# Performance work log

Hardware: AMD Instinct MI355X
Metric: run time of the kernel (lower is better)

Reference implementation:

```python
import jax, jax.numpy as jnp
import numpy as np

FEATURE_SIZES = [300, 1000, 1000, 500, 150, 12, 31, 30, 200, 50000, 50000, 20000, 100000]
# sections per table index i (from feature_sizes_dict -> feature_sections_dict in original)
SECTIONS = [(0, 1), (1, 2), (2, 3), (3, 4), (4, 5), (5, 6), (6, 7), (7, 10),
            (10, 24), (26, 28), (28, 30), (24, 26), (30, 45)]
N, F, E = 8192, 45, 256
_perm, _tbl = [], []
for _i, (_a, _b) in enumerate(SECTIONS):
    for _j in range(_a, _b):
        _perm.append(_j)
        _tbl.append(_i)
PERM = np.array(_perm)              # original Xi column for field position p (concat order)
TBL = np.array(_tbl)                # table index for field position p
OFFSETS = np.concatenate([[0], np.cumsum(FEATURE_SIZES)[:-1]]).astype(np.int32)
FIELD_OFF = OFFSETS[TBL]            # row offset into concatenated table per field position
TOTAL_V = int(np.sum(FEATURE_SIZES))  # 223273
VOCAB_COL = np.zeros(F, np.int32)
VOCAB_COL[PERM] = np.array(FEATURE_SIZES, np.int32)[TBL]  # per-column valid vocab for Xi


def setup_inputs() -> dict:
    key = jax.random.key(0)
    ks = jax.random.split(key, 10)
    Xi = jax.random.randint(ks[0], (N, F), 0, jnp.asarray(VOCAB_COL), dtype=jnp.int32)
    Xv = jax.random.uniform(ks[1], (N, F), dtype=jnp.float32)
    W1 = jax.random.normal(ks[2], (TOTAL_V, 1), dtype=jnp.float32) * 0.01
    W2 = jax.random.normal(ks[3], (TOTAL_V, E), dtype=jnp.float32) * 0.01
    bias = jax.random.normal(ks[4], (1,), dtype=jnp.float32)
    l1_w = jax.random.normal(ks[5], (32, F * E), dtype=jnp.float32) * 0.02
    l1_b = jnp.zeros((32,), jnp.float32)
    l2_w = jax.random.normal(ks[6], (32, 32), dtype=jnp.float32) * 0.02
    l2_b = jnp.zeros((32,), jnp.float32)
    return {"Xi": Xi, "Xv": Xv, "W1": W1, "W2": W2, "bias": bias,
            "l1_w": l1_w, "l1_b": l1_b, "bn1_g": jnp.ones((32,), jnp.float32),
            "bn1_b": jnp.zeros((32,), jnp.float32), "l2_w": l2_w, "l2_b": l2_b,
            "bn2_g": jnp.ones((32,), jnp.float32), "bn2_b": jnp.zeros((32,), jnp.float32)}


def _batchnorm(x, g, b, eps=1e-5):
    # training-mode BN: biased batch statistics (PyTorch normalization convention)
    m = x.mean(0)
    v = x.var(0)
    return (x - m) * jax.lax.rsqrt(v + eps) * g + b


def reference(Xi, Xv, W1, W2, bias, l1_w, l1_b, bn1_g, bn1_b, l2_w, l2_b, bn2_g, bn2_b):
    perm = jnp.asarray(PERM)
    foff = jnp.asarray(FIELD_OFF)
    idx = Xi[:, perm] + foff[None, :]          # (N, 45) rows into concatenated tables
    xv = Xv[:, perm]                            # (N, 45) values in concat order
    # first-order: scalar embedding * value per field
    fm_first = W1[idx, 0] * xv                  # (N, 45)
    # second-order: E-dim embedding * value per field
    e = W2[idx] * xv[:, :, None]                # (N, 45, E)
    s = e.sum(axis=1)                           # (N, E)
    fm_second = 0.5 * (s * s - (e * e).sum(axis=1))  # (N, E)
    # deep part (concat of per-field 2nd-order embs, in original loop order)
    deep = e.reshape(e.shape[0], -1)            # (N, 45*E)
    h = _batchnorm(deep @ l1_w.T + l1_b, bn1_g, bn1_b)
    h = _batchnorm(h @ l2_w.T + l2_b, bn2_g, bn2_b)  # (N, 32); no final num_classes linear in original
    return fm_first.sum(axis=1) + fm_second.sum(axis=1) + h.sum(axis=1) + bias  # (N,)
```

## Files before the change

kernel.cpp:

```cpp
#include <hip/hip_runtime.h>
#include <hip/hip_bf16.h>

#define NS 8192
#define NF 45
#define ED 256
#define L1K 11520
#define NH 32

typedef __attribute__((ext_vector_type(8))) short bf16x8;
typedef __attribute__((ext_vector_type(4))) float f32x4;

__constant__ int c_perm[NF] = {
    0,1,2,3,4,5,6,7,8,9,
    10,11,12,13,14,15,16,17,18,19,20,21,22,23,
    26,27, 28,29, 24,25,
    30,31,32,33,34,35,36,37,38,39,40,41,42,43,44};
__constant__ int c_foff[NF] = {
    0,300,1300,2300,2800,2950,2962,2993,2993,2993,
    3023,3023,3023,3023,3023,3023,3023,3023,3023,3023,3023,3023,3023,3023,
    3223,3223, 53223,53223, 103223,103223,
    123223,123223,123223,123223,123223,123223,123223,123223,
    123223,123223,123223,123223,123223,123223,123223};

__device__ __forceinline__ short f2bf(float x) {
    unsigned u = __builtin_bit_cast(unsigned, x);
    u += 0x7fffu + ((u >> 16) & 1u);
    return (short)(u >> 16);
}

__global__ __launch_bounds__(256) void k_prep(const int* __restrict__ Xi,
                                              const float* __restrict__ Xv,
                                              int* __restrict__ idxP,
                                              float* __restrict__ xvP) {
    int t = blockIdx.x * 256 + threadIdx.x;
    if (t >= NS * NF) return;
    unsigned n = (unsigned)t / NF;
    int f = t - (int)n * NF;
    int col = c_perm[f];
    idxP[t] = Xi[n * NF + col] + c_foff[f];
    xvP[t]  = Xv[n * NF + col];
}

__global__ __launch_bounds__(256) void k_pack(const float* __restrict__ l1w,
                                              short* __restrict__ bfrag) {
    int t = blockIdx.x * 256 + threadIdx.x;
    if (t >= NF * 8192) return;
    int i  = t & 7;
    int l  = (t >> 3) & 63;
    int nt = (t >> 9) & 1;
    int ks = (t >> 10) & 7;
    int f  = t >> 13;
    int kout = nt * 16 + (l & 15);
    int col  = f * 256 + ks * 32 + (l >> 4) * 8 + i;
    bfrag[t] = f2bf(l1w[kout * L1K + col]);
}

__global__ __launch_bounds__(256) void k_main(const float* __restrict__ W2,
                                              const float* __restrict__ W1,
                                              const int* __restrict__ idxP,
                                              const float* __restrict__ xvP,
                                              const short* __restrict__ bfrag,
                                              float* __restrict__ h1pre,
                                              float* __restrict__ partial) {
    __shared__ int   s_idx[16 * NF];
    __shared__ float s_xv [16 * NF];
    __shared__ float s_red[4 * 16 * NH];
    __shared__ float s_q[4][16];
    __shared__ float s_fm1[16];

    const int tid = threadIdx.x;
    const int w = tid >> 6;
    const int l = tid & 63;
    const int m = l & 15;
    const int g4 = l >> 4;
    const int n0 = blockIdx.x * 16;

    for (int t = tid; t < 16 * NF; t += 256) {
        s_idx[t] = idxP[n0 * NF + t];
        s_xv[t]  = xvP [n0 * NF + t];
    }
    __syncthreads();

    const int ks0 = w * 2;
    f32x4 acc0 = {0.f, 0.f, 0.f, 0.f};
    f32x4 acc1 = {0.f, 0.f, 0.f, 0.f};
    float sA[16];
    #pragma unroll
    for (int i = 0; i < 16; ++i) sA[i] = 0.f;
    float esq = 0.f, fm1 = 0.f;

    const short* bbase = bfrag + (size_t)(ks0 * 2) * 512 + l * 8;

    for (int f = 0; f < NF; ++f) {
        const int   idx = s_idx[m * NF + f];
        const float xv  = s_xv [m * NF + f];
        const float* wr = W2 + (size_t)idx * ED + ks0 * 32 + g4 * 8;

        f32x4 a0 = *(const f32x4*)(wr);
        f32x4 a1 = *(const f32x4*)(wr + 4);
        f32x4 a2 = *(const f32x4*)(wr + 32);
        f32x4 a3 = *(const f32x4*)(wr + 36);

        const short* bp = bbase + (size_t)f * 8192;
        bf16x8 b00 = *(const bf16x8*)(bp);
        bf16x8 b01 = *(const bf16x8*)(bp + 512);
        bf16x8 b10 = *(const bf16x8*)(bp + 1024);
        bf16x8 b11 = *(const bf16x8*)(bp + 1536);

        float e[16];
        e[0]=a0.x*xv; e[1]=a0.y*xv; e[2]=a0.z*xv; e[3]=a0.w*xv;
        e[4]=a1.x*xv; e[5]=a1.y*xv; e[6]=a1.z*xv; e[7]=a1.w*xv;
        e[8]=a2.x*xv; e[9]=a2.y*xv; e[10]=a2.z*xv; e[11]=a2.w*xv;
        e[12]=a3.x*xv; e[13]=a3.y*xv; e[14]=a3.z*xv; e[15]=a3.w*xv;

        #pragma unroll
        for (int i = 0; i < 16; ++i) { sA[i] += e[i]; esq += e[i] * e[i]; }

        bf16x8 af0, af1;
        #pragma unroll
        for (int i = 0; i < 8; ++i) { af0[i] = f2bf(e[i]); af1[i] = f2bf(e[8 + i]); }

        acc0 = __builtin_amdgcn_mfma_f32_16x16x32_bf16(af0, b00, acc0, 0, 0, 0);
        acc1 = __builtin_amdgcn_mfma_f32_16x16x32_bf16(af0, b01, acc1, 0, 0, 0);
        acc0 = __builtin_amdgcn_mfma_f32_16x16x32_bf16(af1, b10, acc0, 0, 0, 0);
        acc1 = __builtin_amdgcn_mfma_f32_16x16x32_bf16(af1, b11, acc1, 0, 0, 0);

        if (w == 0) fm1 += W1[idx] * xv;
    }

    float q = -esq;
    #pragma unroll
    for (int i = 0; i < 16; ++i) q += sA[i] * sA[i];
    q += __shfl_xor(q, 16);
    q += __shfl_xor(q, 32);
    if (l < 16) s_q[w][l] = q;
    if (w == 0 && l < 16) s_fm1[l] = fm1;

    #pragma unroll
    for (int r = 0; r < 4; ++r) {
        s_red[w * 512 + (g4 * 4 + r) * 32 +      m] = acc0[r];
        s_red[w * 512 + (g4 * 4 + r) * 32 + 16 + m] = acc1[r];
    }
    __syncthreads();

    for (int t = tid; t < 512; t += 256) {
        float v = s_red[t] + s_red[512 + t] + s_red[1024 + t] + s_red[1536 + t];
        int s = t >> 5, k = t & 31;
        h1pre[(size_t)(n0 + s) * NH + k] = v;
    }
    if (tid < 16) {
        float fm2 = 0.5f * (s_q[0][tid] + s_q[1][tid] + s_q[2][tid] + s_q[3][tid]);
        partial[n0 + tid] = s_fm1[tid] + fm2;
    }
}

__global__ __launch_bounds__(256) void k_stats(const float* __restrict__ h1pre,
                                               float* __restrict__ S1,
                                               float* __restrict__ S2) {
    __shared__ float hc[128 * NH];
    const int tid = threadIdx.x;
    const int base = blockIdx.x * 128;
    for (int t = tid; t < 128 * NH; t += 256) hc[t] = h1pre[(size_t)base * NH + t];
    __syncthreads();

    const int j = tid >> 3;
    const int ks = (tid & 7) * 4;
    float a0 = 0.f, a1 = 0.f, a2 = 0.f, a3 = 0.f;
    for (int n = 0; n < 128; ++n) {
        float hj = hc[n * NH + j];
        f32x4 h = *(const f32x4*)&hc[n * NH + ks];
        a0 += hj * h.x; a1 += hj * h.y; a2 += hj * h.z; a3 += hj * h.w;
    }
    atomicAdd(&S2[j * NH + ks + 0], a0);
    atomicAdd(&S2[j * NH + ks + 1], a1);
    atomicAdd(&S2[j * NH + ks + 2], a2);
    atomicAdd(&S2[j * NH + ks + 3], a3);
    if (tid < NH) {
        float s = 0.f;
        for (int n = 0; n < 128; ++n) s += hc[n * NH + tid];
        atomicAdd(&S1[tid], s);
    }
}

__global__ __launch_bounds__(256) void k_coef(const float* __restrict__ S1,
                                              const float* __restrict__ S2,
                                              const float* __restrict__ g1,
                                              const float* __restrict__ l2w,
                                              const float* __restrict__ g2,
                                              const float* __restrict__ b2,
                                              const float* __restrict__ bias,
                                              float* __restrict__ cvec,
                                              float* __restrict__ k0out) {
    __shared__ float m1[NH], d1[NH], g2r2[NH], csh[NH];
    const int t = threadIdx.x;
    const float invN = 1.f / (float)NS;
    if (t < NH) {
        float mm = S1[t] * invN;
        float v1 = S2[t * NH + t] * invN - mm * mm;
        m1[t] = mm;
        d1[t] = g1[t] * rsqrtf(v1 + 1e-5f);
    }
    __syncthreads();
    if (t < NH) {
        float aw[NH];
        float p = 0.f;
        for (int j = 0; j < NH; ++j) { aw[j] = l2w[t * NH + j] * d1[j]; p += aw[j] * m1[j]; }
        float v2 = 0.f;
        for (int j = 0; j < NH; ++j) {
            float acc = 0.f;
            for (int j2 = 0; j2 < NH; ++j2) acc += aw[j2] * S2[j * NH + j2];
            v2 += aw[j] * acc;
        }
        v2 = v2 * invN - p * p;
        g2r2[t] = g2[t] * rsqrtf(v2 + 1e-5f);
    }
    __syncthreads();
    if (t < NH) {
        float s = 0.f;
        for (int k = 0; k < NH; ++k) s += g2r2[k] * l2w[k * NH + t];
        float c = d1[t] * s;
        csh[t] = c;
        cvec[t] = c;
    }
    __syncthreads();
    if (t == 0) {
        float k0 = bias[0];
        for (int k = 0; k < NH; ++k) k0 += b2[k];
        for (int j = 0; j < NH; ++j) k0 -= csh[j] * m1[j];
        k0out[0] = k0;
    }
}

__global__ __launch_bounds__(256) void k_final(const float* __restrict__ h1pre,
                                               const float* __restrict__ partial,
                                               const float* __restrict__ cvec,
                                               const float* __restrict__ k0p,
                                               float* __restrict__ out) {
    __shared__ float c[NH];
    __shared__ float k0s;
    const int t = threadIdx.x;
    if (t < NH) c[t] = cvec[t];
    if (t == 0) k0s = k0p[0];
    __syncthreads();
    const int n = blockIdx.x * 256 + t;
    const f32x4* hp = (const f32x4*)(h1pre + (size_t)n * NH);
    float dot = 0.f;
    #pragma unroll
    for (int q = 0; q < 8; ++q) {
        f32x4 h = hp[q];
        dot += h.x * c[q * 4] + h.y * c[q * 4 + 1] + h.z * c[q * 4 + 2] + h.w * c[q * 4 + 3];
    }
    out[n] = partial[n] + dot + k0s;
}

extern "C" void kernel_launch(void* const* d_in, const int* in_sizes, int n_in,
                              void* d_out, int out_size, void* d_ws, size_t ws_size,
                              hipStream_t stream) {
    const int*   Xi   = (const int*)  d_in[0];
    const float* Xv   = (const float*)d_in[1];
    const float* W1   = (const float*)d_in[2];
    const float* W2   = (const float*)d_in[3];
    const float* bias = (const float*)d_in[4];
    const float* l1w  = (const float*)d_in[5];
    const float* g1   = (const float*)d_in[7];
    const float* l2w  = (const float*)d_in[9];
    const float* g2   = (const float*)d_in[11];
    const float* b2   = (const float*)d_in[12];
    float* out = (float*)d_out;

    char* ws = (char*)d_ws;
    int*   idxP  = (int*)ws;
    float* xvP   = (float*)(ws + (size_t)368640 * 4);
    short* bfrag = (short*)(ws + (size_t)737280 * 4);
    float* h1    = (float*)(ws + (size_t)737280 * 4 + 737280);
    float* part  = h1 + (size_t)NS * NH;
    float* S1    = part + NS;
    float* S2    = S1 + NH;
    float* cvec  = S2 + NH * NH;
    float* k0p   = cvec + NH;

    hipMemsetAsync(S1, 0, (NH + NH * NH) * sizeof(float), stream);
    k_prep <<<(NS * NF + 255) / 256, 256, 0, stream>>>(Xi, Xv, idxP, xvP);
    k_pack <<<(NF * 8192 + 255) / 256, 256, 0, stream>>>(l1w, bfrag);
    k_main <<<NS / 16, 256, 0, stream>>>(W2, W1, idxP, xvP, bfrag, h1, part);
    k_stats<<<64, 256, 0, stream>>>(h1, S1, S2);
    k_coef <<<1, 256, 0, stream>>>(S1, S2, g1, l2w, g2, b2, bias, cvec, k0p);
    k_final<<<NS / 256, 256, 0, stream>>>(h1, part, cvec, k0p, out);
}
```

Baseline: 392.0 us.

## Fuse index prep into main kernel and split embedding dim across two blocks

Removes the separate k_prep kernel by gathering the permuted indices and values directly inside k_main. The main kernel now launches twice as many blocks, each covering half of the 256-wide embedding dimension, which halves per-thread register and load work and raises occupancy. The two halves write separate partial h1 and FM outputs that k_stats and k_final sum. The cost is redundant index gathering per half-block and extra reads of partial buffers downstream.

```diff
diff --git a/kernel.cpp b/kernel.cpp
--- a/kernel.cpp
+++ b/kernel.cpp
@@ -26,19 +26,6 @@
     unsigned u = __builtin_bit_cast(unsigned, x);
     u += 0x7fffu + ((u >> 16) & 1u);
     return (short)(u >> 16);
-}
-
-__global__ __launch_bounds__(256) void k_prep(const int* __restrict__ Xi,
-                                              const float* __restrict__ Xv,
-                                              int* __restrict__ idxP,
-                                              float* __restrict__ xvP) {
-    int t = blockIdx.x * 256 + threadIdx.x;
-    if (t >= NS * NF) return;
-    unsigned n = (unsigned)t / NF;
-    int f = t - (int)n * NF;
-    int col = c_perm[f];
-    idxP[t] = Xi[n * NF + col] + c_foff[f];
-    xvP[t]  = Xv[n * NF + col];
 }
 
 __global__ __launch_bounds__(256) void k_pack(const float* __restrict__ l1w,
@@ -57,80 +44,77 @@
 
 __global__ __launch_bounds__(256) void k_main(const float* __restrict__ W2,
                                               const float* __restrict__ W1,
-                                              const int* __restrict__ idxP,
-                                              const float* __restrict__ xvP,
+                                              const int* __restrict__ Xi,
+                                              const float* __restrict__ Xv,
                                               const short* __restrict__ bfrag,
-                                              float* __restrict__ h1pre,
-                                              float* __restrict__ partial) {
+                                              float* __restrict__ h1h,
+                                              float* __restrict__ parth) {
     __shared__ int   s_idx[16 * NF];
     __shared__ float s_xv [16 * NF];
     __shared__ float s_red[4 * 16 * NH];
     __shared__ float s_q[4][16];
     __shared__ float s_fm1[16];
 
-    const int tid = threadIdx.x;
-    const int w = tid >> 6;
-    const int l = tid & 63;
-    const int m = l & 15;
-    const int g4 = l >> 4;
-    const int n0 = blockIdx.x * 16;
+    const int tid  = threadIdx.x;
+    const int w    = tid >> 6;
+    const int l    = tid & 63;
+    const int m    = l & 15;
+    const int g4   = l >> 4;
+    const int half = blockIdx.x & 1;
+    const int n0   = (blockIdx.x >> 1) * 16;
+    const int ks   = half * 4 + w;
 
     for (int t = tid; t < 16 * NF; t += 256) {
-        s_idx[t] = idxP[n0 * NF + t];
-        s_xv[t]  = xvP [n0 * NF + t];
-    }
-    __syncthreads();
-
-    const int ks0 = w * 2;
+        int f = t % NF;
+        int n = n0 + t / NF;
+        int col = c_perm[f];
+        s_idx[t] = Xi[n * NF + col] + c_foff[f];
+        s_xv[t]  = Xv[n * NF + col];
+    }
+    __syncthreads();
+
     f32x4 acc0 = {0.f, 0.f, 0.f, 0.f};
     f32x4 acc1 = {0.f, 0.f, 0.f, 0.f};
-    float sA[16];
-    #pragma unroll
-    for (int i = 0; i < 16; ++i) sA[i] = 0.f;
+    float sA[8];
+    #pragma unroll
+    for (int i = 0; i < 8; ++i) sA[i] = 0.f;
     float esq = 0.f, fm1 = 0.f;
 
-    const short* bbase = bfrag + (size_t)(ks0 * 2) * 512 + l * 8;
+    const short* bbase = bfrag + (size_t)ks * 1024 + l * 8;
+    const float* wbase = W2 + ks * 32 + g4 * 8;
 
     for (int f = 0; f < NF; ++f) {
         const int   idx = s_idx[m * NF + f];
         const float xv  = s_xv [m * NF + f];
-        const float* wr = W2 + (size_t)idx * ED + ks0 * 32 + g4 * 8;
+        const float* wr = wbase + (size_t)idx * ED;
 
         f32x4 a0 = *(const f32x4*)(wr);
         f32x4 a1 = *(const f32x4*)(wr + 4);
-        f32x4 a2 = *(const f32x4*)(wr + 32);
-        f32x4 a3 = *(const f32x4*)(wr + 36);
 
         const short* bp = bbase + (size_t)f * 8192;
-        bf16x8 b00 = *(const bf16x8*)(bp);
-        bf16x8 b01 = *(const bf16x8*)(bp + 512);
-        bf16x8 b10 = *(const bf16x8*)(bp + 1024);
-        bf16x8 b11 = *(const bf16x8*)(bp + 1536);
-
-        float e[16];
+        bf16x8 b0 = *(const bf16x8*)(bp);
+        bf16x8 b1 = *(const bf16x8*)(bp + 512);
+
+        float e[8];
         e[0]=a0.x*xv; e[1]=a0.y*xv; e[2]=a0.z*xv; e[3]=a0.w*xv;
         e[4]=a1.x*xv; e[5]=a1.y*xv; e[6]=a1.z*xv; e[7]=a1.w*xv;
-        e[8]=a2.x*xv; e[9]=a2.y*xv; e[10]=a2.z*xv; e[11]=a2.w*xv;
-        e[12]=a3.x*xv; e[13]=a3.y*xv; e[14]=a3.z*xv; e[15]=a3.w*xv;
 
         #pragma unroll
-        for (int i = 0; i < 16; ++i) { sA[i] += e[i]; esq += e[i] * e[i]; }
-
-        bf16x8 af0, af1;
+        for (int i = 0; i < 8; ++i) { sA[i] += e[i]; esq += e[i] * e[i]; }
+
+        bf16x8 af;
         #pragma unroll
-        for (int i = 0; i < 8; ++i) { af0[i] = f2bf(e[i]); af1[i] = f2bf(e[8 + i]); }
-
-        acc0 = __builtin_amdgcn_mfma_f32_16x16x32_bf16(af0, b00, acc0, 0, 0, 0);
-        acc1 = __builtin_amdgcn_mfma_f32_16x16x32_bf16(af0, b01, acc1, 0, 0, 0);
-        acc0 = __builtin_amdgcn_mfma_f32_16x16x32_bf16(af1, b10, acc0, 0, 0, 0);
-        acc1 = __builtin_amdgcn_mfma_f32_16x16x32_bf16(af1, b11, acc1, 0, 0, 0);
-
-        if (w == 0) fm1 += W1[idx] * xv;
+        for (int i = 0; i < 8; ++i) af[i] = f2bf(e[i]);
+
+        acc0 = __builtin_amdgcn_mfma_f32_16x16x32_bf16(af, b0, acc0, 0, 0, 0);
+        acc1 = __builtin_amdgcn_mfma_f32_16x16x32_bf16(af, b1, acc1, 0, 0, 0);
+
+        if (half == 0 && w == 0) fm1 += W1[idx] * xv;
     }
 
     float q = -esq;
     #pragma unroll
-    for (int i = 0; i < 16; ++i) q += sA[i] * sA[i];
+    for (int i = 0; i < 8; ++i) q += sA[i] * sA[i];
     q += __shfl_xor(q, 16);
     q += __shfl_xor(q, 32);
     if (l < 16) s_q[w][l] = q;
@@ -143,24 +127,26 @@
     }
     __syncthreads();
 
+    float* h1out = h1h + (size_t)half * NS * NH;
     for (int t = tid; t < 512; t += 256) {
         float v = s_red[t] + s_red[512 + t] + s_red[1024 + t] + s_red[1536 + t];
         int s = t >> 5, k = t & 31;
-        h1pre[(size_t)(n0 + s) * NH + k] = v;
+        h1out[(size_t)(n0 + s) * NH + k] = v;
     }
     if (tid < 16) {
         float fm2 = 0.5f * (s_q[0][tid] + s_q[1][tid] + s_q[2][tid] + s_q[3][tid]);
-        partial[n0 + tid] = s_fm1[tid] + fm2;
-    }
-}
-
-__global__ __launch_bounds__(256) void k_stats(const float* __restrict__ h1pre,
+        parth[half * NS + n0 + tid] = s_fm1[tid] + fm2;
+    }
+}
+
+__global__ __launch_bounds__(256) void k_stats(const float* __restrict__ h1h,
                                                float* __restrict__ S1,
                                                float* __restrict__ S2) {
     __shared__ float hc[128 * NH];
     const int tid = threadIdx.x;
     const int base = blockIdx.x * 128;
-    for (int t = tid; t < 128 * NH; t += 256) hc[t] = h1pre[(size_t)base * NH + t];
+    for (int t = tid; t < 128 * NH; t += 256)
+        hc[t] = h1h[(size_t)base * NH + t] + h1h[(size_t)NS * NH + base * NH + t];
     __syncthreads();
 
     const int j = tid >> 3;
@@ -231,8 +217,8 @@
     }
 }
 
-__global__ __launch_bounds__(256) void k_final(const float* __restrict__ h1pre,
-                                               const float* __restrict__ partial,
+__global__ __launch_bounds__(256) void k_final(const float* __restrict__ h1h,
+                                               const float* __restrict__ parth,
                                                const float* __restrict__ cvec,
                                                const float* __restrict__ k0p,
                                                float* __restrict__ out) {
@@ -243,14 +229,17 @@
     if (t == 0) k0s = k0p[0];
     __syncthreads();
     const int n = blockIdx.x * 256 + t;
-    const f32x4* hp = (const f32x4*)(h1pre + (size_t)n * NH);
+    const f32x4* hp0 = (const f32x4*)(h1h + (size_t)n * NH);
+    const f32x4* hp1 = (const f32x4*)(h1h + (size_t)NS * NH + (size_t)n * NH);
     float dot = 0.f;
     #pragma unroll
     for (int q = 0; q < 8; ++q) {
-        f32x4 h = hp[q];
-        dot += h.x * c[q * 4] + h.y * c[q * 4 + 1] + h.z * c[q * 4 + 2] + h.w * c[q * 4 + 3];
-    }
-    out[n] = partial[n] + dot + k0s;
+        f32x4 h0 = hp0[q];
+        f32x4 h1 = hp1[q];
+        dot += (h0.x + h1.x) * c[q * 4]     + (h0.y + h1.y) * c[q * 4 + 1]
+             + (h0.z + h1.z) * c[q * 4 + 2] + (h0.w + h1.w) * c[q * 4 + 3];
+    }
+    out[n] = parth[n] + parth[NS + n] + dot + k0s;
 }
 
 extern "C" void kernel_launch(void* const* d_in, const int* in_sizes, int n_in,
@@ -269,21 +258,18 @@
     float* out = (float*)d_out;
 
     char* ws = (char*)d_ws;
-    int*   idxP  = (int*)ws;
-    float* xvP   = (float*)(ws + (size_t)368640 * 4);
-    short* bfrag = (short*)(ws + (size_t)737280 * 4);
-    float* h1    = (float*)(ws + (size_t)737280 * 4 + 737280);
-    float* part  = h1 + (size_t)NS * NH;
-    float* S1    = part + NS;
+    short* bfrag = (short*)ws;
+    float* h1h   = (float*)(ws + (size_t)368640 * 2);
+    float* parth = h1h + (size_t)2 * NS * NH;
+    float* S1    = parth + 2 * NS;
     float* S2    = S1 + NH;
     float* cvec  = S2 + NH * NH;
     float* k0p   = cvec + NH;
 
     hipMemsetAsync(S1, 0, (NH + NH * NH) * sizeof(float), stream);
-    k_prep <<<(NS * NF + 255) / 256, 256, 0, stream>>>(Xi, Xv, idxP, xvP);
     k_pack <<<(NF * 8192 + 255) / 256, 256, 0, stream>>>(l1w, bfrag);
-    k_main <<<NS / 16, 256, 0, stream>>>(W2, W1, idxP, xvP, bfrag, h1, part);
-    k_stats<<<64, 256, 0, stream>>>(h1, S1, S2);
+    k_main <<<NS / 16 * 2, 256, 0, stream>>>(W2, W1, Xi, Xv, bfrag, h1h, parth);
+    k_stats<<<64, 256, 0, stream>>>(h1h, S1, S2);
     k_coef <<<1, 256, 0, stream>>>(S1, S2, g1, l2w, g2, b2, bias, cvec, k0p);
-    k_final<<<NS / 256, 256, 0, stream>>>(h1, part, cvec, k0p, out);
-}
+    k_final<<<NS / 256, 256, 0, stream>>>(h1h, parth, cvec, k0p, out);
+}
```

After: 388.3 us. About the same (-0.9%).

## Fuse prep, stats, coef and final kernels into main pipeline

Applied to the files above, without the earlier changes.

Folds the index/value permutation into k_main's shared-memory load, computes the BN1 moment accumulations (S1/S2) inside k_main via atomics, and merges the coefficient and final-output kernels into one kernel where each block redundantly recomputes the BN coefficients. Zeroing of the accumulators moves into k_pack, and the bf16 conversion uses the packed v_cvt_pk_bf16_f32 instruction. This cuts launch count from six plus a memset down to three and removes intermediate idx/xv buffers. In exchange there are many more atomics (512 blocks instead of 64) and duplicated coefficient work in each of 32 blocks.

```diff
diff --git a/kernel.cpp b/kernel.cpp
--- a/kernel.cpp
+++ b/kernel.cpp
@@ -28,22 +28,19 @@
     return (short)(u >> 16);
 }
 
-__global__ __launch_bounds__(256) void k_prep(const int* __restrict__ Xi,
-                                              const float* __restrict__ Xv,
-                                              int* __restrict__ idxP,
-                                              float* __restrict__ xvP) {
+__device__ __forceinline__ unsigned pk_bf16(float a, float b) {
+    unsigned r;
+    asm("v_cvt_pk_bf16_f32 %0, %1, %2" : "=v"(r) : "v"(a), "v"(b));
+    return r;
+}
+
+__global__ __launch_bounds__(256) void k_pack(const float* __restrict__ l1w,
+                                              short* __restrict__ bfrag,
+                                              float* __restrict__ S1) {
     int t = blockIdx.x * 256 + threadIdx.x;
-    if (t >= NS * NF) return;
-    unsigned n = (unsigned)t / NF;
-    int f = t - (int)n * NF;
-    int col = c_perm[f];
-    idxP[t] = Xi[n * NF + col] + c_foff[f];
-    xvP[t]  = Xv[n * NF + col];
-}
-
-__global__ __launch_bounds__(256) void k_pack(const float* __restrict__ l1w,
-                                              short* __restrict__ bfrag) {
-    int t = blockIdx.x * 256 + threadIdx.x;
+    if (blockIdx.x == 0) {
+        for (int i = threadIdx.x; i < NH + NH * NH; i += 256) S1[i] = 0.f;
+    }
     if (t >= NF * 8192) return;
     int i  = t & 7;
     int l  = (t >> 3) & 63;
@@ -57,14 +54,17 @@
 
 __global__ __launch_bounds__(256) void k_main(const float* __restrict__ W2,
                                               const float* __restrict__ W1,
-                                              const int* __restrict__ idxP,
-                                              const float* __restrict__ xvP,
+                                              const int* __restrict__ Xi,
+                                              const float* __restrict__ Xv,
                                               const short* __restrict__ bfrag,
                                               float* __restrict__ h1pre,
-                                              float* __restrict__ partial) {
+                                              float* __restrict__ partial,
+                                              float* __restrict__ S1,
+                                              float* __restrict__ S2) {
     __shared__ int   s_idx[16 * NF];
     __shared__ float s_xv [16 * NF];
     __shared__ float s_red[4 * 16 * NH];
+    __shared__ float s_h[16 * NH];
     __shared__ float s_q[4][16];
     __shared__ float s_fm1[16];
 
@@ -76,8 +76,11 @@
     const int n0 = blockIdx.x * 16;
 
     for (int t = tid; t < 16 * NF; t += 256) {
-        s_idx[t] = idxP[n0 * NF + t];
-        s_xv[t]  = xvP [n0 * NF + t];
+        int f = t % NF;
+        int n = n0 + t / NF;
+        int col = c_perm[f];
+        s_idx[t] = Xi[n * NF + col] + c_foff[f];
+        s_xv[t]  = Xv[n * NF + col];
     }
     __syncthreads();
 
@@ -116,14 +119,20 @@
         #pragma unroll
         for (int i = 0; i < 16; ++i) { sA[i] += e[i]; esq += e[i] * e[i]; }
 
-        bf16x8 af0, af1;
-        #pragma unroll
-        for (int i = 0; i < 8; ++i) { af0[i] = f2bf(e[i]); af1[i] = f2bf(e[8 + i]); }
-
-        acc0 = __builtin_amdgcn_mfma_f32_16x16x32_bf16(af0, b00, acc0, 0, 0, 0);
-        acc1 = __builtin_amdgcn_mfma_f32_16x16x32_bf16(af0, b01, acc1, 0, 0, 0);
-        acc0 = __builtin_amdgcn_mfma_f32_16x16x32_bf16(af1, b10, acc0, 0, 0, 0);
-        acc1 = __builtin_amdgcn_mfma_f32_16x16x32_bf16(af1, b11, acc1, 0, 0, 0);
+        union { bf16x8 v; unsigned u[4]; } A0, A1;
+        A0.u[0] = pk_bf16(e[0],  e[1]);
+        A0.u[1] = pk_bf16(e[2],  e[3]);
+        A0.u[2] = pk_bf16(e[4],  e[5]);
+        A0.u[3] = pk_bf16(e[6],  e[7]);
+        A1.u[0] = pk_bf16(e[8],  e[9]);
+        A1.u[1] = pk_bf16(e[10], e[11]);
+        A1.u[2] = pk_bf16(e[12], e[13]);
+        A1.u[3] = pk_bf16(e[14], e[15]);
+
+        acc0 = __builtin_amdgcn_mfma_f32_16x16x32_bf16(A0.v, b00, acc0, 0, 0, 0);
+        acc1 = __builtin_amdgcn_mfma_f32_16x16x32_bf16(A0.v, b01, acc1, 0, 0, 0);
+        acc0 = __builtin_amdgcn_mfma_f32_16x16x32_bf16(A1.v, b10, acc0, 0, 0, 0);
+        acc1 = __builtin_amdgcn_mfma_f32_16x16x32_bf16(A1.v, b11, acc1, 0, 0, 0);
 
         if (w == 0) fm1 += W1[idx] * xv;
     }
@@ -145,58 +154,59 @@
 
     for (int t = tid; t < 512; t += 256) {
         float v = s_red[t] + s_red[512 + t] + s_red[1024 + t] + s_red[1536 + t];
-        int s = t >> 5, k = t & 31;
-        h1pre[(size_t)(n0 + s) * NH + k] = v;
+        h1pre[(size_t)n0 * NH + t] = v;
+        s_h[t] = v;
     }
     if (tid < 16) {
         float fm2 = 0.5f * (s_q[0][tid] + s_q[1][tid] + s_q[2][tid] + s_q[3][tid]);
         partial[n0 + tid] = s_fm1[tid] + fm2;
     }
-}
-
-__global__ __launch_bounds__(256) void k_stats(const float* __restrict__ h1pre,
-                                               float* __restrict__ S1,
-                                               float* __restrict__ S2) {
-    __shared__ float hc[128 * NH];
-    const int tid = threadIdx.x;
-    const int base = blockIdx.x * 128;
-    for (int t = tid; t < 128 * NH; t += 256) hc[t] = h1pre[(size_t)base * NH + t];
-    __syncthreads();
-
-    const int j = tid >> 3;
-    const int ks = (tid & 7) * 4;
-    float a0 = 0.f, a1 = 0.f, a2 = 0.f, a3 = 0.f;
-    for (int n = 0; n < 128; ++n) {
-        float hj = hc[n * NH + j];
-        f32x4 h = *(const f32x4*)&hc[n * NH + ks];
-        a0 += hj * h.x; a1 += hj * h.y; a2 += hj * h.z; a3 += hj * h.w;
-    }
-    atomicAdd(&S2[j * NH + ks + 0], a0);
-    atomicAdd(&S2[j * NH + ks + 1], a1);
-    atomicAdd(&S2[j * NH + ks + 2], a2);
-    atomicAdd(&S2[j * NH + ks + 3], a3);
-    if (tid < NH) {
-        float s = 0.f;
-        for (int n = 0; n < 128; ++n) s += hc[n * NH + tid];
-        atomicAdd(&S1[tid], s);
-    }
-}
-
-__global__ __launch_bounds__(256) void k_coef(const float* __restrict__ S1,
-                                              const float* __restrict__ S2,
-                                              const float* __restrict__ g1,
-                                              const float* __restrict__ l2w,
-                                              const float* __restrict__ g2,
-                                              const float* __restrict__ b2,
-                                              const float* __restrict__ bias,
-                                              float* __restrict__ cvec,
-                                              float* __restrict__ k0out) {
+    __syncthreads();
+
+    {
+        const int j  = tid >> 3;
+        const int k4 = (tid & 7) * 4;
+        float a0 = 0.f, a1 = 0.f, a2 = 0.f, a3 = 0.f;
+        #pragma unroll
+        for (int s = 0; s < 16; ++s) {
+            float hj = s_h[s * NH + j];
+            f32x4 h = *(const f32x4*)&s_h[s * NH + k4];
+            a0 += hj * h.x; a1 += hj * h.y; a2 += hj * h.z; a3 += hj * h.w;
+        }
+        atomicAdd(&S2[j * NH + k4 + 0], a0);
+        atomicAdd(&S2[j * NH + k4 + 1], a1);
+        atomicAdd(&S2[j * NH + k4 + 2], a2);
+        atomicAdd(&S2[j * NH + k4 + 3], a3);
+        if (tid < NH) {
+            float s1 = 0.f;
+            #pragma unroll
+            for (int s = 0; s < 16; ++s) s1 += s_h[s * NH + tid];
+            atomicAdd(&S1[tid], s1);
+        }
+    }
+}
+
+__global__ __launch_bounds__(256) void k_cf(const float* __restrict__ S1,
+                                            const float* __restrict__ S2,
+                                            const float* __restrict__ g1,
+                                            const float* __restrict__ l2w,
+                                            const float* __restrict__ g2,
+                                            const float* __restrict__ b2,
+                                            const float* __restrict__ bias,
+                                            const float* __restrict__ h1pre,
+                                            const float* __restrict__ partial,
+                                            float* __restrict__ out) {
+    __shared__ float sS2[NH * NH];
     __shared__ float m1[NH], d1[NH], g2r2[NH], csh[NH];
+    __shared__ float k0s;
     const int t = threadIdx.x;
     const float invN = 1.f / (float)NS;
+
+    for (int i = t; i < NH * NH; i += 256) sS2[i] = S2[i];
+    __syncthreads();
     if (t < NH) {
         float mm = S1[t] * invN;
-        float v1 = S2[t * NH + t] * invN - mm * mm;
+        float v1 = sS2[t * NH + t] * invN - mm * mm;
         m1[t] = mm;
         d1[t] = g1[t] * rsqrtf(v1 + 1e-5f);
     }
@@ -208,7 +218,7 @@
         float v2 = 0.f;
         for (int j = 0; j < NH; ++j) {
             float acc = 0.f;
-            for (int j2 = 0; j2 < NH; ++j2) acc += aw[j2] * S2[j * NH + j2];
+            for (int j2 = 0; j2 < NH; ++j2) acc += aw[j2] * sS2[j * NH + j2];
             v2 += aw[j] * acc;
         }
         v2 = v2 * invN - p * p;
@@ -218,37 +228,25 @@
     if (t < NH) {
         float s = 0.f;
         for (int k = 0; k < NH; ++k) s += g2r2[k] * l2w[k * NH + t];
-        float c = d1[t] * s;
-        csh[t] = c;
-        cvec[t] = c;
+        csh[t] = d1[t] * s;
     }
     __syncthreads();
     if (t == 0) {
         float k0 = bias[0];
         for (int k = 0; k < NH; ++k) k0 += b2[k];
         for (int j = 0; j < NH; ++j) k0 -= csh[j] * m1[j];
-        k0out[0] = k0;
-    }
-}
-
-__global__ __launch_bounds__(256) void k_final(const float* __restrict__ h1pre,
-                                               const float* __restrict__ partial,
-                                               const float* __restrict__ cvec,
-                                               const float* __restrict__ k0p,
-                                               float* __restrict__ out) {
-    __shared__ float c[NH];
-    __shared__ float k0s;
-    const int t = threadIdx.x;
-    if (t < NH) c[t] = cvec[t];
-    if (t == 0) k0s = k0p[0];
-    __syncthreads();
+        k0s = k0;
+    }
+    __syncthreads();
+
     const int n = blockIdx.x * 256 + t;
     const f32x4* hp = (const f32x4*)(h1pre + (size_t)n * NH);
     float dot = 0.f;
     #pragma unroll
     for (int q = 0; q < 8; ++q) {
         f32x4 h = hp[q];
-        dot += h.x * c[q * 4] + h.y * c[q * 4 + 1] + h.z * c[q * 4 + 2] + h.w * c[q * 4 + 3];
+        dot += h.x * csh[q * 4] + h.y * csh[q * 4 + 1]
+             + h.z * csh[q * 4 + 2] + h.w * csh[q * 4 + 3];
     }
     out[n] = partial[n] + dot + k0s;
 }
@@ -269,21 +267,13 @@
     float* out = (float*)d_out;
 
     char* ws = (char*)d_ws;
-    int*   idxP  = (int*)ws;
-    float* xvP   = (float*)(ws + (size_t)368640 * 4);
-    short* bfrag = (short*)(ws + (size_t)737280 * 4);
-    float* h1    = (float*)(ws + (size_t)737280 * 4 + 737280);
+    short* bfrag = (short*)ws;
+    float* h1    = (float*)(ws + (size_t)368640 * 2);
     float* part  = h1 + (size_t)NS * NH;
     float* S1    = part + NS;
     float* S2    = S1 + NH;
-    float* cvec  = S2 + NH * NH;
-    float* k0p   = cvec + NH;
-
-    hipMemsetAsync(S1, 0, (NH + NH * NH) * sizeof(float), stream);
-    k_prep <<<(NS * NF + 255) / 256, 256, 0, stream>>>(Xi, Xv, idxP, xvP);
-    k_pack <<<(NF * 8192 + 255) / 256, 256, 0, stream>>>(l1w, bfrag);
-    k_main <<<NS / 16, 256, 0, stream>>>(W2, W1, idxP, xvP, bfrag, h1, part);
-    k_stats<<<64, 256, 0, stream>>>(h1, S1, S2);
-    k_coef <<<1, 256, 0, stream>>>(S1, S2, g1, l2w, g2, b2, bias, cvec, k0p);
-    k_final<<<NS / 256, 256, 0, stream>>>(h1, part, cvec, k0p, out);
-}
+
+    k_pack<<<(NF * 8192 + 255) / 256, 256, 0, stream>>>(l1w, bfrag, S1);
+    k_main<<<NS / 16, 256, 0, stream>>>(W2, W1, Xi, Xv, bfrag, h1, part, S1, S2);
+    k_cf  <<<NS / 256, 256, 0, stream>>>(S1, S2, g1, l2w, g2, b2, bias, h1, part, out);
+}
```

Measured after the change: 412.5 us. +5.2%, slower.

## Stage gathered embeddings in LDS with double-buffered chunks and fuse prep into main

Applied to the files above, without the earlier changes.

The prep kernel is removed and its index permutation and offset work moves into k_main's prologue. Embedding rows are now gathered with fully coalesced 1KB row reads (one row per wave-iteration). Each row is scaled, converted to bf16 and written into a double-buffered LDS tile two fields at a time, and the MFMA loop reads its A fragments from LDS while the next chunk is prefetched. The aim is to replace scattered per-lane 32-byte gathers with contiguous row reads and overlap gather latency with compute. In exchange it adds a block barrier per phase, more LDS use, and computes the FM second-order sums from bf16-rounded values, which loses some precision.

```diff
diff --git a/kernel.cpp b/kernel.cpp
--- a/kernel.cpp
+++ b/kernel.cpp
@@ -6,6 +6,10 @@
 #define ED 256
 #define L1K 11520
 #define NH 32
+#define CHUNK 2
+#define NPH 23
+#define ROWSTRIDE 264
+#define FSTRIDE (16 * ROWSTRIDE)
 
 typedef __attribute__((ext_vector_type(8))) short bf16x8;
 typedef __attribute__((ext_vector_type(4))) float f32x4;
@@ -28,17 +32,17 @@
     return (short)(u >> 16);
 }
 
-__global__ __launch_bounds__(256) void k_prep(const int* __restrict__ Xi,
-                                              const float* __restrict__ Xv,
-                                              int* __restrict__ idxP,
-                                              float* __restrict__ xvP) {
-    int t = blockIdx.x * 256 + threadIdx.x;
-    if (t >= NS * NF) return;
-    unsigned n = (unsigned)t / NF;
-    int f = t - (int)n * NF;
-    int col = c_perm[f];
-    idxP[t] = Xi[n * NF + col] + c_foff[f];
-    xvP[t]  = Xv[n * NF + col];
+__device__ __forceinline__ unsigned pk_bf16(float a, float b) {
+    unsigned r;
+    asm("v_cvt_pk_bf16_f32 %0, %1, %2" : "=v"(r) : "v"(a), "v"(b));
+    return r;
+}
+
+__device__ __forceinline__ float bfu_lo(unsigned u) {
+    return __builtin_bit_cast(float, (unsigned)(u << 16));
+}
+__device__ __forceinline__ float bfu_hi(unsigned u) {
+    return __builtin_bit_cast(float, (unsigned)(u & 0xffff0000u));
 }
 
 __global__ __launch_bounds__(256) void k_pack(const float* __restrict__ l1w,
@@ -57,75 +61,121 @@
 
 __global__ __launch_bounds__(256) void k_main(const float* __restrict__ W2,
                                               const float* __restrict__ W1,
-                                              const int* __restrict__ idxP,
-                                              const float* __restrict__ xvP,
+                                              const int* __restrict__ Xi,
+                                              const float* __restrict__ Xv,
                                               const short* __restrict__ bfrag,
                                               float* __restrict__ h1pre,
                                               float* __restrict__ partial) {
     __shared__ int   s_idx[16 * NF];
     __shared__ float s_xv [16 * NF];
-    __shared__ float s_red[4 * 16 * NH];
+    __shared__ short s_e[2][CHUNK * FSTRIDE];
+    __shared__ float s_red[4 * 512];
     __shared__ float s_q[4][16];
     __shared__ float s_fm1[16];
 
     const int tid = threadIdx.x;
-    const int w = tid >> 6;
-    const int l = tid & 63;
-    const int m = l & 15;
-    const int g4 = l >> 4;
-    const int n0 = blockIdx.x * 16;
-
+    const int w   = tid >> 6;
+    const int l   = tid & 63;
+    const int m   = l & 15;
+    const int g4  = l >> 4;
+    const int n0  = blockIdx.x * 16;
+
+    if (tid < 16) s_fm1[tid] = 0.f;
     for (int t = tid; t < 16 * NF; t += 256) {
-        s_idx[t] = idxP[n0 * NF + t];
-        s_xv[t]  = xvP [n0 * NF + t];
-    }
-    __syncthreads();
-
-    const int ks0 = w * 2;
+        int f = t % NF;
+        int n = n0 + t / NF;
+        int col = c_perm[f];
+        s_idx[t] = Xi[n * NF + col] + c_foff[f];
+        s_xv[t]  = Xv[n * NF + col];
+    }
+    __syncthreads();
+
     f32x4 acc0 = {0.f, 0.f, 0.f, 0.f};
     f32x4 acc1 = {0.f, 0.f, 0.f, 0.f};
     float sA[16];
     #pragma unroll
     for (int i = 0; i < 16; ++i) sA[i] = 0.f;
-    float esq = 0.f, fm1 = 0.f;
-
-    const short* bbase = bfrag + (size_t)(ks0 * 2) * 512 + l * 8;
-
-    for (int f = 0; f < NF; ++f) {
-        const int   idx = s_idx[m * NF + f];
-        const float xv  = s_xv [m * NF + f];
-        const float* wr = W2 + (size_t)idx * ED + ks0 * 32 + g4 * 8;
-
-        f32x4 a0 = *(const f32x4*)(wr);
-        f32x4 a1 = *(const f32x4*)(wr + 4);
-        f32x4 a2 = *(const f32x4*)(wr + 32);
-        f32x4 a3 = *(const f32x4*)(wr + 36);
-
-        const short* bp = bbase + (size_t)f * 8192;
-        bf16x8 b00 = *(const bf16x8*)(bp);
-        bf16x8 b01 = *(const bf16x8*)(bp + 512);
-        bf16x8 b10 = *(const bf16x8*)(bp + 1024);
-        bf16x8 b11 = *(const bf16x8*)(bp + 1536);
-
-        float e[16];
-        e[0]=a0.x*xv; e[1]=a0.y*xv; e[2]=a0.z*xv; e[3]=a0.w*xv;
-        e[4]=a1.x*xv; e[5]=a1.y*xv; e[6]=a1.z*xv; e[7]=a1.w*xv;
-        e[8]=a2.x*xv; e[9]=a2.y*xv; e[10]=a2.z*xv; e[11]=a2.w*xv;
-        e[12]=a3.x*xv; e[13]=a3.y*xv; e[14]=a3.z*xv; e[15]=a3.w*xv;
-
+    float esq = 0.f;
+
+    {
+        const int nrows = 16 * CHUNK;
         #pragma unroll
-        for (int i = 0; i < 16; ++i) { sA[i] += e[i]; esq += e[i] * e[i]; }
-
-        bf16x8 af0, af1;
-        #pragma unroll
-        for (int i = 0; i < 8; ++i) { af0[i] = f2bf(e[i]); af1[i] = f2bf(e[8 + i]); }
-
-        acc0 = __builtin_amdgcn_mfma_f32_16x16x32_bf16(af0, b00, acc0, 0, 0, 0);
-        acc1 = __builtin_amdgcn_mfma_f32_16x16x32_bf16(af0, b01, acc1, 0, 0, 0);
-        acc0 = __builtin_amdgcn_mfma_f32_16x16x32_bf16(af1, b10, acc0, 0, 0, 0);
-        acc1 = __builtin_amdgcn_mfma_f32_16x16x32_bf16(af1, b11, acc1, 0, 0, 0);
-
-        if (w == 0) fm1 += W1[idx] * xv;
+        for (int j = 0; j < 8; ++j) {
+            int rr = w * 8 + j;
+            int fi = rr >> 4;
+            int mm = rr & 15;
+            int f  = fi;
+            int idx  = s_idx[mm * NF + f];
+            float xv = s_xv [mm * NF + f];
+            f32x4 a = *(const f32x4*)(W2 + (size_t)idx * ED + l * 4);
+            if (l == 0) atomicAdd(&s_fm1[mm], W1[idx] * xv);
+            uint2 v;
+            v.x = pk_bf16(a.x * xv, a.y * xv);
+            v.y = pk_bf16(a.z * xv, a.w * xv);
+            *(uint2*)(&s_e[0][fi * FSTRIDE + mm * ROWSTRIDE + l * 4]) = v;
+            (void)nrows;
+        }
+    }
+    __syncthreads();
+
+    for (int p = 0; p < NPH; ++p) {
+        const int cur = p & 1;
+
+        if (p + 1 < NPH) {
+            const int pn = p + 1;
+            const int nf = (pn * CHUNK + CHUNK <= NF) ? CHUNK : (NF - pn * CHUNK);
+            const int nrows = nf * 16;
+            #pragma unroll
+            for (int j = 0; j < 8; ++j) {
+                int rr = w * 8 + j;
+                if (rr < nrows) {
+                    int fi = rr >> 4;
+                    int mm = rr & 15;
+                    int f  = pn * CHUNK + fi;
+                    int idx  = s_idx[mm * NF + f];
+                    float xv = s_xv [mm * NF + f];
+                    f32x4 a = *(const f32x4*)(W2 + (size_t)idx * ED + l * 4);
+                    if (l == 0) atomicAdd(&s_fm1[mm], W1[idx] * xv);
+                    uint2 v;
+                    v.x = pk_bf16(a.x * xv, a.y * xv);
+                    v.y = pk_bf16(a.z * xv, a.w * xv);
+                    *(uint2*)(&s_e[cur ^ 1][fi * FSTRIDE + mm * ROWSTRIDE + l * 4]) = v;
+                }
+            }
+        }
+
+        {
+            const int nf = (p * CHUNK + CHUNK <= NF) ? CHUNK : (NF - p * CHUNK);
+            #pragma unroll
+            for (int fi = 0; fi < CHUNK; ++fi) {
+                if (fi < nf) {
+                    const int f = p * CHUNK + fi;
+                    #pragma unroll
+                    for (int kk = 0; kk < 2; ++kk) {
+                        const int ks = w * 2 + kk;
+                        bf16x8 af = *(const bf16x8*)
+                            (&s_e[cur][fi * FSTRIDE + m * ROWSTRIDE + ks * 32 + g4 * 8]);
+                        const short* bp = bfrag + (size_t)f * 8192 + ks * 1024 + l * 8;
+                        bf16x8 b0 = *(const bf16x8*)(bp);
+                        bf16x8 b1 = *(const bf16x8*)(bp + 512);
+
+                        union { bf16x8 v; unsigned u[4]; } A;
+                        A.v = af;
+                        #pragma unroll
+                        for (int d = 0; d < 4; ++d) {
+                            float elo = bfu_lo(A.u[d]);
+                            float ehi = bfu_hi(A.u[d]);
+                            sA[kk * 8 + 2 * d]     += elo;
+                            sA[kk * 8 + 2 * d + 1] += ehi;
+                            esq += elo * elo + ehi * ehi;
+                        }
+                        acc0 = __builtin_amdgcn_mfma_f32_16x16x32_bf16(af, b0, acc0, 0, 0, 0);
+                        acc1 = __builtin_amdgcn_mfma_f32_16x16x32_bf16(af, b1, acc1, 0, 0, 0);
+                    }
+                }
+            }
+        }
+        __syncthreads();
     }
 
     float q = -esq;
@@ -134,7 +184,6 @@
     q += __shfl_xor(q, 16);
     q += __shfl_xor(q, 32);
     if (l < 16) s_q[w][l] = q;
-    if (w == 0 && l < 16) s_fm1[l] = fm1;
 
     #pragma unroll
     for (int r = 0; r < 4; ++r) {
@@ -145,8 +194,7 @@
 
     for (int t = tid; t < 512; t += 256) {
         float v = s_red[t] + s_red[512 + t] + s_red[1024 + t] + s_red[1536 + t];
-        int s = t >> 5, k = t & 31;
-        h1pre[(size_t)(n0 + s) * NH + k] = v;
+        h1pre[(size_t)n0 * NH + t] = v;
     }
     if (tid < 16) {
         float fm2 = 0.5f * (s_q[0][tid] + s_q[1][tid] + s_q[2][tid] + s_q[3][tid]);
@@ -269,10 +317,8 @@
     float* out = (float*)d_out;
 
     char* ws = (char*)d_ws;
-    int*   idxP  = (int*)ws;
-    float* xvP   = (float*)(ws + (size_t)368640 * 4);
-    short* bfrag = (short*)(ws + (size_t)737280 * 4);
-    float* h1    = (float*)(ws + (size_t)737280 * 4 + 737280);
+    short* bfrag = (short*)ws;
+    float* h1    = (float*)(ws + (size_t)368640 * 2);
     float* part  = h1 + (size_t)NS * NH;
     float* S1    = part + NS;
     float* S2    = S1 + NH;
@@ -280,9 +326,8 @@
     float* k0p   = cvec + NH;
 
     hipMemsetAsync(S1, 0, (NH + NH * NH) * sizeof(float), stream);
-    k_prep <<<(NS * NF + 255) / 256, 256, 0, stream>>>(Xi, Xv, idxP, xvP);
     k_pack <<<(NF * 8192 + 255) / 256, 256, 0, stream>>>(l1w, bfrag);
-    k_main <<<NS / 16, 256, 0, stream>>>(W2, W1, idxP, xvP, bfrag, h1, part);
+    k_main <<<NS / 16, 256, 0, stream>>>(W2, W1, Xi, Xv, bfrag, h1, part);
     k_stats<<<64, 256, 0, stream>>>(h1, S1, S2);
     k_coef <<<1, 256, 0, stream>>>(S1, S2, g1, l2w, g2, b2, bias, cvec, k0p);
     k_final<<<NS / 256, 256, 0, stream>>>(h1, part, cvec, k0p, out);
```

After: 413.7 us. 5.5% more time.
